# Optimization experiments

Measured on AMD Instinct MI355X. Metric: run time of the kernel, lower is better.

## Reference

```python
import jax, jax.numpy as jnp
import numpy as np

TEMPERATURE = 0.07
EPS = 1e-12  # F.normalize eps


def _construct_labels(visual_ids, anchor_idx):
    # Faithful vectorization of the original order-dependent double loop:
    # for i < B-1: final write to labels[i] comes from pair (i, B-1)
    #   -> 1 iff ids[i]==anchor_id and ids[B-1]==anchor_id, else 0
    # for i == B-1: final write comes from pair (B-2, B-1)
    #   -> 1 iff ids[B-1]==anchor_id and ids[B-2]==anchor_id, else 0
    B = visual_ids.shape[0]
    anchor_id = visual_ids[anchor_idx]
    same = visual_ids == anchor_id  # [B] bool
    labels = jnp.where(same & same[B - 1], 1, 0).astype(jnp.int32)
    labels = labels.at[B - 1].set((same[B - 1] & same[B - 2]).astype(jnp.int32))
    return labels


def setup_inputs() -> dict:
    key = jax.random.key(0)
    k1, k2 = jax.random.split(key)
    visual_feat = jax.random.normal(k1, (8192, 512), dtype=jnp.float32)
    visual_ids = jax.random.randint(k2, (8192,), 0, 1024, dtype=jnp.int64 if jax.config.jax_enable_x64 else jnp.int32)
    anchor_idx = 3
    return {"visual_feat": visual_feat, "visual_ids": visual_ids, "anchor_idx": anchor_idx}


def reference(visual_feat, visual_ids, anchor_idx):
    # L2 normalize rows (F.normalize: x / max(||x||, eps))
    norm = jnp.sqrt(jnp.sum(visual_feat * visual_feat, axis=1, keepdims=True))
    f = visual_feat / jnp.maximum(norm, EPS)
    sim = jnp.matmul(f, f.T) / TEMPERATURE  # [B, B]
    labels = _construct_labels(visual_ids, anchor_idx)  # [B] int in {0,1}
    logp = jax.nn.log_softmax(sim, axis=-1)  # [B, B]
    picked = jnp.take_along_axis(logp, labels[:, None], axis=1)[:, 0]
    loss = -jnp.mean(picked)
    return loss
```

## Files before the change

### kernel.cpp

```cpp
#include <hip/hip_runtime.h>


typedef int i32x8 __attribute__((ext_vector_type(8)));
typedef float f32x4 __attribute__((ext_vector_type(4)));

#define B_N 8192
#define D_K 512
#define ROWB 512
#define INVT 14.285714285714286f
#define SCALE_LOG2 20.609929155556622f

#if defined(__has_builtin) && __has_builtin(__builtin_amdgcn_exp2f)
#define FAST_EXP2(x) __builtin_amdgcn_exp2f(x)
#else
#define FAST_EXP2(x) exp2f(x)
#endif

union FragU {
  int4 h[2];
  i32x8 v;
};

static __device__ __forceinline__ void load16_to_lds(const void* g, void* l) {
  __builtin_amdgcn_global_load_lds(
      (const __attribute__((address_space(1))) unsigned int*)g,
      (__attribute__((address_space(3))) unsigned int*)l, 16, 0, 0);
}

__global__ __launch_bounds__(256)
void norm_kernel(const float* __restrict__ x,
                 unsigned char* __restrict__ fQ,
                 float* __restrict__ Z) {
  const int row = blockIdx.x * 4 + (threadIdx.x >> 6);
  const int lane = threadIdx.x & 63;
  const float4* xr = (const float4*)(x + (size_t)row * D_K);
  float4 a = xr[2 * lane];
  float4 b = xr[2 * lane + 1];
  float s = a.x * a.x + a.y * a.y + a.z * a.z + a.w * a.w +
            b.x * b.x + b.y * b.y + b.z * b.z + b.w * b.w;
#pragma unroll
  for (int off = 1; off < 64; off <<= 1) s += __shfl_xor(s, off);
  const float inv = 1.0f / fmaxf(sqrtf(s), 1e-12f);
  int lo = 0, hi = 0;
  lo = __builtin_amdgcn_cvt_pk_fp8_f32(a.x * inv, a.y * inv, lo, false);
  lo = __builtin_amdgcn_cvt_pk_fp8_f32(a.z * inv, a.w * inv, lo, true);
  hi = __builtin_amdgcn_cvt_pk_fp8_f32(b.x * inv, b.y * inv, hi, false);
  hi = __builtin_amdgcn_cvt_pk_fp8_f32(b.z * inv, b.w * inv, hi, true);
  int2 p; p.x = lo; p.y = hi;
  ((int2*)(fQ + (size_t)row * ROWB))[lane] = p;
  if (lane == 0) Z[row] = 0.0f;
}

__global__ __launch_bounds__(256, 2)
void sim_kernel(const unsigned char* __restrict__ fQ,
                float* __restrict__ Z, float* __restrict__ T01,
                float* __restrict__ D) {
  __shared__ unsigned char ldsA[4][128 * 128];
  __shared__ unsigned char ldsB[128 * 128];

  const int tid = threadIdx.x;
  const int lane = tid & 63;
  const int w = tid >> 6;
  const int wm = w & 1;
  const int wn = w >> 1;
  const int bx = blockIdx.x, by = blockIdx.y;
  const int b = by & 7;
  const int I = (by < 8) ? bx : (63 - bx);
  const int Jfirst = I + ((b - I) & 7);
  if (Jfirst > 63) return;
  const int I0 = I * 128;

  const int srow = lane >> 3;
  const int sb = lane & 7;
  const int su = sb ^ srow;
  const int sg = 2 * (su & 3) + (su >> 2);
  const size_t sOff = (size_t)srow * ROWB + sg * 16;

  const int fr = lane & 15;
  const int q = lane >> 4;
  const int swz = fr & 7;

  const int raRow = (wm * 64 + fr) * 128;
  const unsigned char* rbBase = ldsB + (wn * 64 + fr) * 128;
  const int off0 = (q ^ swz) * 16;
  const int off1 = ((q + 4) ^ swz) * 16;

#pragma unroll
  for (int kk = 0; kk < 4; ++kk) {
    const unsigned char* gA = fQ + (size_t)(I0 + w * 32) * ROWB + kk * 128 + sOff;
    unsigned char* lA = ldsA[kk] + (w * 32) * 128;
#pragma unroll
    for (int rr = 0; rr < 32; rr += 8)
      load16_to_lds(gA + (size_t)rr * ROWB, lA + rr * 128);
  }

  float Zp[4][4];
#pragma unroll
  for (int m = 0; m < 4; ++m)
#pragma unroll
    for (int r = 0; r < 4; ++r) Zp[m][r] = 0.0f;

#pragma unroll 1
  for (int J = Jfirst; J < 64; J += 8) {
    const int J0 = J * 128;
    f32x4 acc[4][4];
#pragma unroll
    for (int m = 0; m < 4; ++m)
#pragma unroll
      for (int n = 0; n < 4; ++n) acc[m][n] = (f32x4){0.f, 0.f, 0.f, 0.f};

#pragma unroll 1
    for (int kk = 0; kk < 4; ++kk) {
      const int k0 = kk * 128;
      {
        const unsigned char* gB = fQ + (size_t)(J0 + w * 32) * ROWB + k0 + sOff;
        unsigned char* lB = ldsB + (w * 32) * 128;
#pragma unroll
        for (int rr = 0; rr < 32; rr += 8)
          load16_to_lds(gB + (size_t)rr * ROWB, lB + rr * 128);
      }
      __syncthreads();

      const unsigned char* raBase = ldsA[kk] + raRow;
      i32x8 bv[4];
#pragma unroll
      for (int n = 0; n < 4; ++n) {
        const unsigned char* rb = rbBase + n * 16 * 128;
        FragU u;
        u.h[0] = *(const int4*)(rb + off0);
        u.h[1] = *(const int4*)(rb + off1);
        bv[n] = u.v;
      }
#pragma unroll
      for (int mh = 0; mh < 2; ++mh) {
        i32x8 av[2];
#pragma unroll
        for (int m = 0; m < 2; ++m) {
          const unsigned char* ra = raBase + (mh * 2 + m) * 16 * 128;
          FragU u;
          u.h[0] = *(const int4*)(ra + off0);
          u.h[1] = *(const int4*)(ra + off1);
          av[m] = u.v;
        }
#pragma unroll
        for (int m = 0; m < 2; ++m)
#pragma unroll
          for (int n = 0; n < 4; ++n)
            acc[mh * 2 + m][n] = __builtin_amdgcn_mfma_scale_f32_16x16x128_f8f6f4(
                av[m], bv[n], acc[mh * 2 + m][n], 0, 0, 0, 127, 0, 127);
      }
      __syncthreads();
    }

    if (I == 0 && wm == 0) {
      if (q == 0) {
#pragma unroll
        for (int n = 0; n < 4; ++n) {
          const int col = J0 + wn * 64 + n * 16 + fr;
          T01[col * 2 + 0] = acc[0][n][0] * INVT;
          T01[col * 2 + 1] = acc[0][n][1] * INVT;
        }
      }
    }

    if (J == I) {
#pragma unroll
      for (int m = 0; m < 4; ++m)
#pragma unroll
        for (int n = 0; n < 4; ++n) {
          const int col = J0 + wn * 64 + n * 16 + fr;
#pragma unroll
          for (int r = 0; r < 4; ++r) {
            const int row = I0 + wm * 64 + m * 16 + q * 4 + r;
            if (row == col) D[row] = acc[m][n][r];
          }
        }
    }

    const bool offd = (J != I);
#pragma unroll
    for (int n = 0; n < 4; ++n) {
      float cs = 0.0f;
#pragma unroll
      for (int m = 0; m < 4; ++m)
#pragma unroll
        for (int r = 0; r < 4; ++r) {
          const float e = FAST_EXP2((acc[m][n][r] - 1.0f) * SCALE_LOG2);
          Zp[m][r] += e;
          cs += e;
        }
      if (offd) {
        cs += __shfl_xor(cs, 16);
        cs += __shfl_xor(cs, 32);
        if (q == 0) atomicAdd(&Z[J0 + wn * 64 + n * 16 + fr], cs);
      }
    }
  }

#pragma unroll
  for (int m = 0; m < 4; ++m)
#pragma unroll
    for (int r = 0; r < 4; ++r) {
      float v = Zp[m][r];
      v += __shfl_xor(v, 1);
      v += __shfl_xor(v, 2);
      v += __shfl_xor(v, 4);
      v += __shfl_xor(v, 8);
      if (fr == 0) atomicAdd(&Z[I0 + wm * 64 + m * 16 + q * 4 + r], v);
    }
}

__global__ __launch_bounds__(1024)
void finalize_kernel(const float* __restrict__ Z,
                     const float* __restrict__ T01,
                     const float* __restrict__ D,
                     const int* __restrict__ ids,
                     const int* __restrict__ anchor,
                     float* __restrict__ out) {
  __shared__ float red[1024];
  const int t = threadIdx.x;
  const int anchor_id = ids[anchor[0]];
  const int sameLast = (ids[B_N - 1] == anchor_id);
  const int samePrev = (ids[B_N - 2] == anchor_id);
  int i[8], id[8];
  float z[8], d[8], t0[8], t1[8];
#pragma unroll
  for (int u = 0; u < 8; ++u) {
    i[u] = u * 1024 + t;
    z[u] = Z[i[u]];
    d[u] = D[i[u]];
    t0[u] = T01[i[u] * 2 + 0];
    t1[u] = T01[i[u] * 2 + 1];
    id[u] = ids[i[u]];
  }
  float sum = 0.0f;
#pragma unroll
  for (int u = 0; u < 8; ++u) {
    const int same_i = (id[u] == anchor_id);
    const int lab =
        (i[u] < B_N - 1) ? (same_i & sameLast) : (sameLast & samePrev);
    const float tt = lab ? t1[u] : t0[u];
    const float Zc = z[u] - FAST_EXP2((d[u] - 1.0f) * SCALE_LOG2) + 1.0f;
    sum += tt - (INVT + logf(Zc));
  }
  red[t] = sum;
  __syncthreads();
  for (int off = 512; off > 0; off >>= 1) {
    if (t < off) red[t] += red[t + off];
    __syncthreads();
  }
  if (t == 0) out[0] = -red[0] / (float)B_N;
}

extern "C" void kernel_launch(void* const* d_in, const int* in_sizes, int n_in,
                              void* d_out, int out_size, void* d_ws, size_t ws_size,
                              hipStream_t stream) {
  const float* x = (const float*)d_in[0];
  const int* ids = (const int*)d_in[1];
  const int* anchor = (const int*)d_in[2];
  float* out = (float*)d_out;

  unsigned char* fQ = (unsigned char*)d_ws;
  float* Z = (float*)((char*)d_ws + (size_t)B_N * ROWB);
  float* T01 = Z + B_N;
  float* D = T01 + 2 * B_N;

  norm_kernel<<<B_N / 4, 256, 0, stream>>>(x, fQ, Z);
  sim_kernel<<<dim3(32, 16), 256, 0, stream>>>(fQ, Z, T01, D);
  finalize_kernel<<<1, 1024, 0, stream>>>(Z, T01, D, ids, anchor, out);
}
```

Before: 104.4 us.

## Split sim kernel into 64-row blocks with per-wave independent B slabs

Reworks the symmetric similarity kernel so each block owns a 64-row A slab shared by all waves, while each wave streams its own 64-column B slab into private LDS. This removes the block-wide __syncthreads inside the K loop, replacing them with a per-wave waitcnt, and doubles the grid so the triangular work is spread over more blocks. In exchange the A tile is reused less per block, global traffic for B rises, and per-wave LDS load/compute ordering now depends only on vmcnt waits.

```diff
diff --git a/kernel.cpp b/kernel.cpp
--- a/kernel.cpp
+++ b/kernel.cpp
@@ -55,20 +55,19 @@
 void sim_kernel(const unsigned char* __restrict__ fQ,
                 float* __restrict__ Z, float* __restrict__ T01,
                 float* __restrict__ D) {
-  __shared__ unsigned char ldsA[4][128 * 128];
-  __shared__ unsigned char ldsB[128 * 128];
+  __shared__ unsigned char ldsA[4][64 * 128];
+  __shared__ unsigned char ldsB[4][64 * 128];
 
   const int tid = threadIdx.x;
   const int lane = tid & 63;
   const int w = tid >> 6;
-  const int wm = w & 1;
-  const int wn = w >> 1;
   const int bx = blockIdx.x, by = blockIdx.y;
-  const int b = by & 7;
-  const int I = (by < 8) ? bx : (63 - bx);
-  const int Jfirst = I + ((b - I) & 7);
-  if (Jfirst > 63) return;
-  const int I0 = I * 128;
+  const int I = (by < 8) ? bx : (127 - bx);
+  const int c = by & 7;
+  const int Jmin = I >> 2;
+  const int Jfirst = Jmin + ((c - Jmin) & 7);
+  if (Jfirst > 31) return;
+  const int I0 = I * 64;
 
   const int srow = lane >> 3;
   const int sb = lane & 7;
@@ -79,20 +78,22 @@
   const int fr = lane & 15;
   const int q = lane >> 4;
   const int swz = fr & 7;
-
-  const int raRow = (wm * 64 + fr) * 128;
-  const unsigned char* rbBase = ldsB + (wn * 64 + fr) * 128;
   const int off0 = (q ^ swz) * 16;
   const int off1 = ((q + 4) ^ swz) * 16;
 
 #pragma unroll
   for (int kk = 0; kk < 4; ++kk) {
-    const unsigned char* gA = fQ + (size_t)(I0 + w * 32) * ROWB + kk * 128 + sOff;
-    unsigned char* lA = ldsA[kk] + (w * 32) * 128;
-#pragma unroll
-    for (int rr = 0; rr < 32; rr += 8)
+    const unsigned char* gA = fQ + (size_t)(I0 + w * 16) * ROWB + kk * 128 + sOff;
+    unsigned char* lA = ldsA[kk] + (w * 16) * 128;
+#pragma unroll
+    for (int rr = 0; rr < 16; rr += 8)
       load16_to_lds(gA + (size_t)rr * ROWB, lA + rr * 128);
   }
+  __syncthreads();
+
+  unsigned char* myB = ldsB[w];
+  const unsigned char* rbBase = myB + fr * 128;
+  const int raRow = fr * 128;
 
   float Zp[4][4];
 #pragma unroll
@@ -101,8 +102,11 @@
     for (int r = 0; r < 4; ++r) Zp[m][r] = 0.0f;
 
 #pragma unroll 1
-  for (int J = Jfirst; J < 64; J += 8) {
-    const int J0 = J * 128;
+  for (int Jg = Jfirst; Jg < 32; Jg += 8) {
+    const int slabCol = 4 * Jg + w;
+    if (slabCol < I) continue;
+    const int J0 = slabCol * 64;
+
     f32x4 acc[4][4];
 #pragma unroll
     for (int m = 0; m < 4; ++m)
@@ -113,13 +117,12 @@
     for (int kk = 0; kk < 4; ++kk) {
       const int k0 = kk * 128;
       {
-        const unsigned char* gB = fQ + (size_t)(J0 + w * 32) * ROWB + k0 + sOff;
-        unsigned char* lB = ldsB + (w * 32) * 128;
-#pragma unroll
-        for (int rr = 0; rr < 32; rr += 8)
-          load16_to_lds(gB + (size_t)rr * ROWB, lB + rr * 128);
-      }
-      __syncthreads();
+        const unsigned char* gB = fQ + (size_t)J0 * ROWB + k0 + sOff;
+#pragma unroll
+        for (int rr = 0; rr < 64; rr += 8)
+          load16_to_lds(gB + (size_t)rr * ROWB, myB + rr * 128);
+      }
+      __builtin_amdgcn_s_waitcnt(0x0f70);
 
       const unsigned char* raBase = ldsA[kk] + raRow;
       i32x8 bv[4];
@@ -149,35 +152,32 @@
             acc[mh * 2 + m][n] = __builtin_amdgcn_mfma_scale_f32_16x16x128_f8f6f4(
                 av[m], bv[n], acc[mh * 2 + m][n], 0, 0, 0, 127, 0, 127);
       }
-      __syncthreads();
-    }
-
-    if (I == 0 && wm == 0) {
-      if (q == 0) {
+    }
+
+    if (I == 0 && q == 0) {
+#pragma unroll
+      for (int n = 0; n < 4; ++n) {
+        const int col = J0 + n * 16 + fr;
+        T01[col * 2 + 0] = acc[0][n][0] * INVT;
+        T01[col * 2 + 1] = acc[0][n][1] * INVT;
+      }
+    }
+
+    if (slabCol == I) {
+#pragma unroll
+      for (int m = 0; m < 4; ++m)
 #pragma unroll
         for (int n = 0; n < 4; ++n) {
-          const int col = J0 + wn * 64 + n * 16 + fr;
-          T01[col * 2 + 0] = acc[0][n][0] * INVT;
-          T01[col * 2 + 1] = acc[0][n][1] * INVT;
-        }
-      }
-    }
-
-    if (J == I) {
-#pragma unroll
-      for (int m = 0; m < 4; ++m)
-#pragma unroll
-        for (int n = 0; n < 4; ++n) {
-          const int col = J0 + wn * 64 + n * 16 + fr;
+          const int colL = n * 16 + fr;
 #pragma unroll
           for (int r = 0; r < 4; ++r) {
-            const int row = I0 + wm * 64 + m * 16 + q * 4 + r;
-            if (row == col) D[row] = acc[m][n][r];
+            const int rowL = m * 16 + q * 4 + r;
+            if (rowL == colL) D[I0 + rowL] = acc[m][n][r];
           }
         }
     }
 
-    const bool offd = (J != I);
+    const bool offd = (slabCol != I);
 #pragma unroll
     for (int n = 0; n < 4; ++n) {
       float cs = 0.0f;
@@ -192,7 +192,7 @@
       if (offd) {
         cs += __shfl_xor(cs, 16);
         cs += __shfl_xor(cs, 32);
-        if (q == 0) atomicAdd(&Z[J0 + wn * 64 + n * 16 + fr], cs);
+        if (q == 0) atomicAdd(&Z[J0 + n * 16 + fr], cs);
       }
     }
   }
@@ -206,7 +206,7 @@
       v += __shfl_xor(v, 2);
       v += __shfl_xor(v, 4);
       v += __shfl_xor(v, 8);
-      if (fr == 0) atomicAdd(&Z[I0 + wm * 64 + m * 16 + q * 4 + r], v);
+      if (fr == 0) atomicAdd(&Z[I0 + m * 16 + q * 4 + r], v);
     }
 }
 
@@ -266,6 +266,6 @@
   float* D = T01 + 2 * B_N;
 
   norm_kernel<<<B_N / 4, 256, 0, stream>>>(x, fQ, Z);
-  sim_kernel<<<dim3(32, 16), 256, 0, stream>>>(fQ, Z, T01, D);
+  sim_kernel<<<dim3(64, 16), 256, 0, stream>>>(fQ, Z, T01, D);
   finalize_kernel<<<1, 1024, 0, stream>>>(Z, T01, D, ids, anchor, out);
 }
```

Result: no change. 105.3 us (+0.9%).
